# Performance work log

Hardware: AMD Instinct MI355X
Metric: run time of the kernel (lower is better)

The kernel has to match this reference:

```python
import jax, jax.numpy as jnp
import numpy as np
from jax import lax

B, N, NPOINT, NSAMPLE = 8, 8192, 2048, 32
RADIUS = 0.2
D_FEAT = 64
MLP = [64, 64, 128]
IN_CH = 3 + D_FEAT
EPS = 1e-5


def setup_inputs() -> dict:
    key = jax.random.key(0)
    ks = jax.random.split(key, 2 + len(MLP))
    inp = {
        "xyz": jax.random.uniform(ks[0], (B, N, 3), dtype=jnp.float32),
        "points": jax.random.normal(ks[1], (B, N, D_FEAT), dtype=jnp.float32),
    }
    cin = IN_CH
    for i, cout in enumerate(MLP):
        inp[f"W{i+1}"] = jax.random.normal(ks[2 + i], (cout, cin), dtype=jnp.float32) * 0.05
        inp[f"b{i+1}"] = jnp.zeros((cout,), jnp.float32)
        inp[f"g{i+1}"] = jnp.ones((cout,), jnp.float32)
        inp[f"be{i+1}"] = jnp.zeros((cout,), jnp.float32)
        cin = cout
    return inp


def farthest_point_sample(xyz, npoint):
    # xyz: (B, N, 3) -> (B, npoint) int32 indices. Deterministic start at index 0.
    Bb, Nn, _ = xyz.shape
    barange = jnp.arange(Bb)

    def step(carry, _):
        distance, farthest = carry
        centroid = xyz[barange, farthest]                      # (B, 3)
        d = jnp.sum((xyz - centroid[:, None, :]) ** 2, -1)     # (B, N)
        distance = jnp.minimum(distance, d)
        new_far = jnp.argmax(distance, axis=-1).astype(jnp.int32)
        return (distance, new_far), farthest

    init = (jnp.full((Bb, Nn), 1e10, xyz.dtype), jnp.zeros((Bb,), jnp.int32))
    _, idxs = lax.scan(step, init, None, length=npoint)        # (npoint, B)
    return idxs.T                                              # (B, npoint)


def index_points(points, idx):
    # points: (B, N, C); idx: (B, S) or (B, S, K)
    return jax.vmap(lambda p, i: p[i])(points, idx)


def square_distance(src, dst):
    # (B, S, C) x (B, N, C) -> (B, S, N)
    d = -2.0 * jnp.einsum('bsc,bnc->bsn', src, dst)
    d += jnp.sum(src ** 2, -1)[:, :, None]
    d += jnp.sum(dst ** 2, -1)[:, None, :]
    return d


def query_ball_point(radius, nsample, xyz, new_xyz):
    Bb, Nn, _ = xyz.shape
    sqr = square_distance(new_xyz, xyz)                        # (B, S, N)
    grid = jnp.arange(Nn, dtype=jnp.int32)
    group_idx = jnp.where(sqr > radius * radius, Nn, grid)     # invalid -> N
    # nsample smallest indices == torch sort(dim=-1)[:, :, :nsample]
    neg_vals, _ = lax.top_k(-group_idx, nsample)               # (B, S, K)
    group_idx = -neg_vals
    first = group_idx[:, :, 0:1]
    return jnp.where(group_idx == Nn, first, group_idx)


def bn_relu(x, gamma, beta):
    # x: (B, C, L). Training-mode batchnorm (biased variance) + ReLU.
    mean = jnp.mean(x, axis=(0, 2), keepdims=True)
    var = jnp.mean((x - mean) ** 2, axis=(0, 2), keepdims=True)
    xn = (x - mean) * lax.rsqrt(var + EPS)
    return jax.nn.relu(xn * gamma[None, :, None] + beta[None, :, None])


def reference(xyz, points, W1, b1, g1, be1, W2, b2, g2, be2, W3, b3, g3, be3):
    Bb = xyz.shape[0]
    fps_idx = farthest_point_sample(xyz, NPOINT)               # (B, S)
    new_xyz = index_points(xyz, fps_idx)                       # (B, S, 3)
    idx = query_ball_point(RADIUS, NSAMPLE, xyz, new_xyz)      # (B, S, K)
    grouped_xyz = index_points(xyz, idx)                       # (B, S, K, 3)
    grouped_xyz_norm = grouped_xyz - new_xyz[:, :, None, :]
    grouped_points = index_points(points, idx)                 # (B, S, K, D)
    g = jnp.concatenate([grouped_xyz_norm, grouped_points], -1)  # (B, S, K, C)
    x = g.reshape(Bb, NPOINT * NSAMPLE, -1).transpose(0, 2, 1)   # (B, C, S*K)
    for W, b, ga, be in ((W1, b1, g1, be1), (W2, b2, g2, be2), (W3, b3, g3, be3)):
        x = jnp.einsum('oc,bcl->bol', W, x) + b[None, :, None]
        x = bn_relu(x, ga, be)
    x = x.reshape(Bb, -1, NPOINT, NSAMPLE)
    new_points = jnp.max(x, axis=-1).transpose(0, 2, 1)        # (B, S, C_out)
    return new_xyz, new_points
```

## Files before the change

kernel.cpp:

```cpp
#include <hip/hip_runtime.h>
#include <hip/hip_bf16.h>

#define NB 8
#define NN 8192
#define NP 2048
#define NS 32
#define INV_P (1.0f/524288.0f)

typedef float v2f __attribute__((ext_vector_type(2)));

template<int CTRL>
__device__ __forceinline__ float fmax_dpp(float v) {
  const int x = __builtin_amdgcn_update_dpp(0, __float_as_int(v), CTRL, 0xF, 0xF, true);
  return fmaxf(v, __int_as_float(x));
}


__global__ __launch_bounds__(512)
void k_fps_pre(const float* __restrict__ xyz, const float* __restrict__ feat,
               const float* __restrict__ W1, const float* __restrict__ b1,
               float* __restrict__ F, float* __restrict__ outXyz, float* __restrict__ stats)
{
#pragma clang fp contract(off)
  __shared__ union U { float4 xyzw[NN]; float fx[128*64]; } sh;
  __shared__ unsigned long long cand[2][8];
  __shared__ float ctrs[3*NP];
  const int t = threadIdx.x;
  if (blockIdx.x < 8) {
    const int b = blockIdx.x;
    const float* xb = xyz + (size_t)b*NN*3;
    v2f px[8], py[8], pz[8], dd[8];
#pragma unroll
    for (int j = 0; j < 8; ++j) {
      const int i0 = t*16 + 2*j;
      const float x0 = xb[i0*3+0], y0 = xb[i0*3+1], z0 = xb[i0*3+2];
      const float x1 = xb[i0*3+3], y1 = xb[i0*3+4], z1 = xb[i0*3+5];
      px[j] = (v2f){x0,x1}; py[j] = (v2f){y0,y1}; pz[j] = (v2f){z0,z1};
      dd[j] = (v2f){1e10f,1e10f};
      sh.xyzw[i0]   = make_float4(x0,y0,z0,0.f);
      sh.xyzw[i0+1] = make_float4(x1,y1,z1,0.f);
    }
    __syncthreads();
    const int lane = t & 63, wv = t >> 6;
    float4 cf = sh.xyzw[0];
    for (int s = 0; s < NP; ++s) {
      if (t == 0) { ctrs[s] = cf.x; ctrs[NP+s] = cf.y; ctrs[2*NP+s] = cf.z; }
      const v2f cx = {cf.x,cf.x}, cy = {cf.y,cf.y}, cz = {cf.z,cf.z};
      v2f mxv = {-1.f,-1.f};
#pragma unroll
      for (int j = 0; j < 8; ++j) {
        const v2f dx = px[j]-cx, dy = py[j]-cy, dz = pz[j]-cz;
        v2f d = dx*dx; d = d + dy*dy; d = d + dz*dz;
        const v2f nd = __builtin_elementwise_min(dd[j], d);
        dd[j] = nd;
        mxv = __builtin_elementwise_max(mxv, nd);
      }
      float m = fmaxf(mxv.x, mxv.y);
      float r = m;
      r = fmax_dpp<0xB1>(r);
      r = fmax_dpp<0x4E>(r);
      r = fmax_dpp<0x141>(r);
      r = fmax_dpp<0x140>(r);
      r = fmax_dpp<0x142>(r);
      r = fmax_dpp<0x143>(r);
      const int wmb  = __builtin_amdgcn_readlane(__float_as_int(r), 63);
      const float wm = __int_as_float(wmb);
      const unsigned long long mk = __ballot(m == wm);
      const int ls = __ffsll((long long)mk) - 1;
      if (lane == ls) {
        int k = 0;
#pragma unroll
        for (int j = 7; j >= 0; --j) {
          if (dd[j].y == wm) k = 2*j+1;
          if (dd[j].x == wm) k = 2*j;
        }
        const unsigned idx = (unsigned)(t*16 + k);
        cand[s&1][wv] = ((unsigned long long)(unsigned)wmb << 32)
                      | (unsigned long long)(0xFFFFFFFFu - idx);
      }
      __syncthreads();
      unsigned long long best = cand[s&1][0];
#pragma unroll
      for (int w = 1; w < 8; ++w) { const unsigned long long c = cand[s&1][w]; if (c > best) best = c; }
      const int far = (int)(0xFFFFFFFFu - (unsigned)(best & 0xFFFFFFFFull));
      cf = sh.xyzw[far];
    }
    for (int i = t; i < NP; i += 512) {
      float* o = outXyz + ((size_t)b*NP + i)*3;
      o[0] = ctrs[i]; o[1] = ctrs[NP+i]; o[2] = ctrs[2*NP+i];
    }
  } else {
    if (blockIdx.x == 8) {
      for (int i = t; i < 512*16; i += 512) stats[i] = 0.f;
    }
    const int blk = blockIdx.x - 8;
    const int base = blk * 128;
    const int b = base >> 13;
    const int n0 = base & (NN-1);
    {
      const int row = t >> 2, seg = t & 3;
      const float* src = feat + ((size_t)(b*NN + n0 + row))*64 + seg*16;
#pragma unroll
      for (int k = 0; k < 4; ++k) {
        const float4 v = *(const float4*)(src + k*4);
        *(float4*)&sh.fx[row*64 + seg*16 + k*4] = v;
      }
    }
    __syncthreads();
    const int o = t & 63, wv = t >> 6;
    float w[64];
#pragma unroll
    for (int c = 0; c < 64; ++c) w[c] = W1[o*67 + 3 + c];
    const float bb = b1[o];
    for (int r = wv*16; r < wv*16+16; ++r) {
      float acc = bb;
#pragma unroll
      for (int c4 = 0; c4 < 16; ++c4) {
        const float4 xq = *(const float4*)&sh.fx[r*64 + c4*4];
        acc = fmaf(w[c4*4+0], xq.x, acc);
        acc = fmaf(w[c4*4+1], xq.y, acc);
        acc = fmaf(w[c4*4+2], xq.z, acc);
        acc = fmaf(w[c4*4+3], xq.w, acc);
      }
      F[((size_t)(b*NN + n0 + r))*64 + o] = acc;
    }
  }
}

__global__ __launch_bounds__(256)
void k_ball(const float* __restrict__ xyz, const float* __restrict__ newXyz,
            const float* __restrict__ F, const float* __restrict__ W1,
            __hip_bfloat16* __restrict__ y1, float* __restrict__ stats)
{
  __shared__ float xs[NN], ys[NN], zs[NN];
  __shared__ int sel[4][NS];
  const int t = threadIdx.x;
  const int b = blockIdx.x >> 5;
  const int chunk = blockIdx.x & 31;
  const float* xb = xyz + (size_t)b*NN*3;
  for (int i = t; i < NN; i += 256) {
    xs[i] = xb[i*3+0]; ys[i] = xb[i*3+1]; zs[i] = xb[i*3+2];
  }
  __syncthreads();
  const int lane = t & 63, wv = t >> 6;
  const float w0 = W1[lane*67+0], w1 = W1[lane*67+1], w2 = W1[lane*67+2];
  const double rr = 0.2*0.2;
  float ls = 0.f, lq = 0.f;
  for (int qi = 0; qi < 16; ++qi) {
    const int q  = chunk*64 + wv*16 + qi;
    const int gq = b*NP + q;
    const float cx = newXyz[(size_t)gq*3+0], cy = newXyz[(size_t)gq*3+1], cz = newXyz[(size_t)gq*3+2];
    const double cxd = (double)cx, cyd = (double)cy, czd = (double)cz;
    const double ssd = cxd*cxd + cyd*cyd + czd*czd;
    int have = 0;
    for (int c0 = 0; c0 < NN; c0 += 64) {
      const int i = c0 + lane;
      const double x = (double)xs[i], y = (double)ys[i], z = (double)zs[i];
      const double dot = x*cxd + y*cyd + z*czd;
      const double pn2 = x*x + y*y + z*z;
      const double d = -2.0*dot + ssd + pn2;
      const bool ok = d <= rr;
      const unsigned long long mk = __ballot(ok);
      const int rank = __popcll(mk & ((1ull<<lane)-1ull));
      if (ok && have + rank < NS) sel[wv][have+rank] = i;
      have += (int)__popcll(mk);
      if (have >= NS) break;
    }
    if (have > NS) have = NS;
    const int first = sel[wv][0];
    if (lane >= have && lane < NS) sel[wv][lane] = first;
    for (int j = 0; j < NS; ++j) {
      const int i = sel[wv][j];
      const float dxn = xs[i]-cx, dyn = ys[i]-cy, dzn = zs[i]-cz;
      const float f = F[((size_t)(b*NN+i))*64 + lane];
      float yv = fmaf(w0,dxn,f); yv = fmaf(w1,dyn,yv); yv = fmaf(w2,dzn,yv);
      y1[((size_t)gq*NS + j)*64 + lane] = __float2bfloat16(yv);
      ls += yv; lq = fmaf(yv,yv,lq);
    }
  }
  atomicAdd(&stats[(0 +lane)*16], ls);
  atomicAdd(&stats[(64+lane)*16], lq);
}

__device__ inline void stage_bn(const __hip_bfloat16* __restrict__ src, float* __restrict__ xt,
                                const float* __restrict__ A, const float* __restrict__ Bc,
                                int t, int blockBase)
{
  const uint4* s = (const uint4*)(src + ((size_t)(blockBase + t))*64);
  float* row = &xt[t*64];
  const int sw = t & 7;
#pragma unroll
  for (int g = 0; g < 8; ++g) {
    const uint4 v = s[g];
    const unsigned uu[4] = {v.x, v.y, v.z, v.w};
    const float4 Aq0 = ((const float4*)A)[g*2],  Aq1 = ((const float4*)A)[g*2+1];
    const float4 Bq0 = ((const float4*)Bc)[g*2], Bq1 = ((const float4*)Bc)[g*2+1];
    float e[8];
#pragma unroll
    for (int k = 0; k < 4; ++k) {
      const float f0 = __uint_as_float(uu[k] << 16);
      const float f1 = __uint_as_float(uu[k] & 0xFFFF0000u);
      const float a0 = (k<2) ? ((k==0)?Aq0.x:Aq0.z) : ((k==2)?Aq1.x:Aq1.z);
      const float a1 = (k<2) ? ((k==0)?Aq0.y:Aq0.w) : ((k==2)?Aq1.y:Aq1.w);
      const float bb0 = (k<2) ? ((k==0)?Bq0.x:Bq0.z) : ((k==2)?Bq1.x:Bq1.z);
      const float bb1 = (k<2) ? ((k==0)?Bq0.y:Bq0.w) : ((k==2)?Bq1.y:Bq1.w);
      e[k*2+0] = fmaxf(fmaf(f0, a0, bb0), 0.f);
      e[k*2+1] = fmaxf(fmaf(f1, a1, bb1), 0.f);
    }
    const float4 q0 = make_float4(e[0],e[1],e[2],e[3]);
    const float4 q1 = make_float4(e[4],e[5],e[6],e[7]);
    ((float4*)row)[(g*2)   ^ sw] = q0;
    ((float4*)row)[(g*2+1) ^ sw] = q1;
  }
}

__global__ __launch_bounds__(256)
void k_l2(const __hip_bfloat16* __restrict__ y1, float* __restrict__ stats,
          const float* __restrict__ g1, const float* __restrict__ be1,
          const float* __restrict__ W2, const float* __restrict__ b2,
          __hip_bfloat16* __restrict__ y2)
{
  __shared__ float xt[256*64];
  __shared__ float A[64], Bc[64], ssh[64], qsh[64];
  const int t = threadIdx.x;
  if (t < 64) {
    const float mean = stats[t*16] * INV_P;
    float var = stats[(64+t)*16] * INV_P - mean*mean;
    if (var < 0.f) var = 0.f;
    const float rs = rsqrtf(var + 1e-5f);
    const float a = rs * g1[t];
    A[t] = a; Bc[t] = fmaf(-mean, a, be1[t]);
    ssh[t] = 0.f; qsh[t] = 0.f;
  }
  const int lane = t & 63, wv = t >> 6;
  float w[64];
#pragma unroll
  for (int c4 = 0; c4 < 16; ++c4) {
    const float4 v = *(const float4*)(W2 + lane*64 + c4*4);
    w[c4*4+0]=v.x; w[c4*4+1]=v.y; w[c4*4+2]=v.z; w[c4*4+3]=v.w;
  }
  const float bo = b2[lane];
  __syncthreads();
  stage_bn(y1, xt, A, Bc, t, blockIdx.x*256);
  __syncthreads();
  float ls = 0.f, lq = 0.f;
  for (int pp = 0; pp < 64; ++pp) {
    const int p = wv*64 + pp;
    const int sw = p & 7;
    const float* row = &xt[p*64];
    float acc = bo;
#pragma unroll
    for (int c4 = 0; c4 < 16; ++c4) {
      const float4 xq = ((const float4*)row)[c4 ^ sw];
      acc = fmaf(w[c4*4+0], xq.x, acc);
      acc = fmaf(w[c4*4+1], xq.y, acc);
      acc = fmaf(w[c4*4+2], xq.z, acc);
      acc = fmaf(w[c4*4+3], xq.w, acc);
    }
    y2[((size_t)(blockIdx.x*256 + p))*64 + lane] = __float2bfloat16(acc);
    ls += acc; lq = fmaf(acc,acc,lq);
  }
  atomicAdd(&ssh[lane], ls);
  atomicAdd(&qsh[lane], lq);
  __syncthreads();
  if (t < 64) {
    atomicAdd(&stats[(128+t)*16], ssh[t]);
    atomicAdd(&stats[(192+t)*16], qsh[t]);
  }
}

__global__ __launch_bounds__(256)
void k_l3stats(const __hip_bfloat16* __restrict__ y2, float* __restrict__ stats,
               const float* __restrict__ g2, const float* __restrict__ be2,
               const float* __restrict__ W3, const float* __restrict__ b3)
{
  __shared__ float xt[256*64];
  __shared__ float A[64], Bc[64], ssh[128], qsh[128];
  const int t = threadIdx.x;
  if (t < 64) {
    const float mean = stats[(128+t)*16] * INV_P;
    float var = stats[(192+t)*16] * INV_P - mean*mean;
    if (var < 0.f) var = 0.f;
    const float rs = rsqrtf(var + 1e-5f);
    const float a = rs * g2[t];
    A[t] = a; Bc[t] = fmaf(-mean, a, be2[t]);
  }
  if (t < 128) { ssh[t]=0.f; qsh[t]=0.f; }
  const int lane = t & 63, wv = t >> 6;
  float w0[64], w1[64];
#pragma unroll
  for (int c4 = 0; c4 < 16; ++c4) {
    const float4 v  = *(const float4*)(W3 + lane*64 + c4*4);
    const float4 v2 = *(const float4*)(W3 + (size_t)(lane+64)*64 + c4*4);
    w0[c4*4+0]=v.x;  w0[c4*4+1]=v.y;  w0[c4*4+2]=v.z;  w0[c4*4+3]=v.w;
    w1[c4*4+0]=v2.x; w1[c4*4+1]=v2.y; w1[c4*4+2]=v2.z; w1[c4*4+3]=v2.w;
  }
  const float bo0 = b3[lane], bo1 = b3[lane+64];
  __syncthreads();
  stage_bn(y2, xt, A, Bc, t, blockIdx.x*256);
  __syncthreads();
  float ls0=0.f,lq0=0.f,ls1=0.f,lq1=0.f;
  for (int pp = 0; pp < 64; ++pp) {
    const int p = wv*64 + pp;
    const int sw = p & 7;
    const float* row = &xt[p*64];
    float a0 = bo0, a1 = bo1;
#pragma unroll
    for (int c4 = 0; c4 < 16; ++c4) {
      const float4 xq = ((const float4*)row)[c4 ^ sw];
      a0 = fmaf(w0[c4*4+0], xq.x, a0); a0 = fmaf(w0[c4*4+1], xq.y, a0);
      a0 = fmaf(w0[c4*4+2], xq.z, a0); a0 = fmaf(w0[c4*4+3], xq.w, a0);
      a1 = fmaf(w1[c4*4+0], xq.x, a1); a1 = fmaf(w1[c4*4+1], xq.y, a1);
      a1 = fmaf(w1[c4*4+2], xq.z, a1); a1 = fmaf(w1[c4*4+3], xq.w, a1);
    }
    ls0 += a0; lq0 = fmaf(a0,a0,lq0);
    ls1 += a1; lq1 = fmaf(a1,a1,lq1);
  }
  atomicAdd(&ssh[lane], ls0);    atomicAdd(&qsh[lane], lq0);
  atomicAdd(&ssh[64+lane], ls1); atomicAdd(&qsh[64+lane], lq1);
  __syncthreads();
  if (t < 128) {
    atomicAdd(&stats[(256+t)*16], ssh[t]);
    atomicAdd(&stats[(384+t)*16], qsh[t]);
  }
}

__global__ __launch_bounds__(256)
void k_out(const __hip_bfloat16* __restrict__ y2, const float* __restrict__ stats,
           const float* __restrict__ g2, const float* __restrict__ be2,
           const float* __restrict__ W3, const float* __restrict__ b3,
           const float* __restrict__ g3, const float* __restrict__ be3,
           float* __restrict__ out)
{
  __shared__ float xt[256*64];
  __shared__ float A[64], Bc[64], A3[128], B3[128];
  const int t = threadIdx.x;
  if (t < 64) {
    const float mean = stats[(128+t)*16] * INV_P;
    float var = stats[(192+t)*16] * INV_P - mean*mean;
    if (var < 0.f) var = 0.f;
    const float rs = rsqrtf(var + 1e-5f);
    const float a = rs * g2[t];
    A[t] = a; Bc[t] = fmaf(-mean, a, be2[t]);
  }
  if (t < 128) {
    const float mean = stats[(256+t)*16] * INV_P;
    float var = stats[(384+t)*16] * INV_P - mean*mean;
    if (var < 0.f) var = 0.f;
    const float rs = rsqrtf(var + 1e-5f);
    const float a = rs * g3[t];
    A3[t] = a; B3[t] = fmaf(-mean, a, be3[t]);
  }
  const int lane = t & 63, wv = t >> 6;
  float w0[64], w1[64];
#pragma unroll
  for (int c4 = 0; c4 < 16; ++c4) {
    const float4 v  = *(const float4*)(W3 + lane*64 + c4*4);
    const float4 v2 = *(const float4*)(W3 + (size_t)(lane+64)*64 + c4*4);
    w0[c4*4+0]=v.x;  w0[c4*4+1]=v.y;  w0[c4*4+2]=v.z;  w0[c4*4+3]=v.w;
    w1[c4*4+0]=v2.x; w1[c4*4+1]=v2.y; w1[c4*4+2]=v2.z; w1[c4*4+3]=v2.w;
  }
  const float bo0 = b3[lane], bo1 = b3[lane+64];
  __syncthreads();
  stage_bn(y2, xt, A, Bc, t, blockIdx.x*256);
  __syncthreads();
  const float a3l0 = A3[lane], b3l0 = B3[lane];
  const float a3l1 = A3[64+lane], b3l1 = B3[64+lane];
  for (int which = 0; which < 2; ++which) {
    float mx0 = -1e30f, mx1 = -1e30f;
    for (int j = 0; j < 32; ++j) {
      const int p = (wv*2+which)*32 + j;
      const int sw = p & 7;
      const float* row = &xt[p*64];
      float a0 = bo0, a1 = bo1;
#pragma unroll
      for (int c4 = 0; c4 < 16; ++c4) {
        const float4 xq = ((const float4*)row)[c4 ^ sw];
        a0 = fmaf(w0[c4*4+0], xq.x, a0); a0 = fmaf(w0[c4*4+1], xq.y, a0);
        a0 = fmaf(w0[c4*4+2], xq.z, a0); a0 = fmaf(w0[c4*4+3], xq.w, a0);
        a1 = fmaf(w1[c4*4+0], xq.x, a1); a1 = fmaf(w1[c4*4+1], xq.y, a1);
        a1 = fmaf(w1[c4*4+2], xq.z, a1); a1 = fmaf(w1[c4*4+3], xq.w, a1);
      }
      mx0 = fmaxf(mx0, fmaf(a0, a3l0, b3l0));
      mx1 = fmaxf(mx1, fmaf(a1, a3l1, b3l1));
    }
    const size_t gq = (size_t)blockIdx.x*8 + wv*2 + which;
    out[49152 + gq*128 + lane]      = fmaxf(mx0, 0.f);
    out[49152 + gq*128 + 64 + lane] = fmaxf(mx1, 0.f);
  }
}

extern "C" void kernel_launch(void* const* d_in, const int* in_sizes, int n_in,
                              void* d_out, int out_size, void* d_ws, size_t ws_size,
                              hipStream_t stream)
{
  const float* xyz = (const float*)d_in[0];
  const float* pts = (const float*)d_in[1];
  const float* W1  = (const float*)d_in[2];
  const float* b1  = (const float*)d_in[3];
  const float* g1  = (const float*)d_in[4];
  const float* be1 = (const float*)d_in[5];
  const float* W2  = (const float*)d_in[6];
  const float* b2_ = (const float*)d_in[7];
  const float* g2  = (const float*)d_in[8];
  const float* be2 = (const float*)d_in[9];
  const float* W3  = (const float*)d_in[10];
  const float* b3_ = (const float*)d_in[11];
  const float* g3  = (const float*)d_in[12];
  const float* be3 = (const float*)d_in[13];
  float* out = (float*)d_out;
  char* ws = (char*)d_ws;

  float* stats = (float*)(ws);
  float* F     = (float*)(ws + (1u<<20));
  __hip_bfloat16* y1 = (__hip_bfloat16*)(ws + (32u<<20));
  __hip_bfloat16* y2 = (__hip_bfloat16*)(ws + (112u<<20));

  k_fps_pre<<<520, 512, 0, stream>>>(xyz, pts, W1, b1, F, out, stats);
  k_ball<<<256, 256, 0, stream>>>(xyz, out, F, W1, y1, stats);
  k_l2<<<2048, 256, 0, stream>>>(y1, stats, g1, be1, W2, b2_, y2);
  k_l3stats<<<2048, 256, 0, stream>>>(y2, stats, g2, be2, W3, b3_);
  k_out<<<2048, 256, 0, stream>>>(y2, stats, g2, be2, W3, b3_, g3, be3, out);
}
```

Baseline: 2.505 ms.

## Shrink FPS block to four waves with 32 points per thread and winner coordinates

```diff
diff --git a/kernel.cpp b/kernel.cpp
--- a/kernel.cpp
+++ b/kernel.cpp
@@ -16,23 +16,24 @@
 }
 
 
-__global__ __launch_bounds__(512)
+__global__ __launch_bounds__(256)
 void k_fps_pre(const float* __restrict__ xyz, const float* __restrict__ feat,
                const float* __restrict__ W1, const float* __restrict__ b1,
                float* __restrict__ F, float* __restrict__ outXyz, float* __restrict__ stats)
 {
 #pragma clang fp contract(off)
-  __shared__ union U { float4 xyzw[NN]; float fx[128*64]; } sh;
-  __shared__ unsigned long long cand[2][8];
+  __shared__ union U { float4 xyzw[NN]; float fx[64*64]; } sh;
+  __shared__ unsigned long long skey[2][4];
+  __shared__ float4 scrd[2][4];
   __shared__ float ctrs[3*NP];
   const int t = threadIdx.x;
   if (blockIdx.x < 8) {
     const int b = blockIdx.x;
     const float* xb = xyz + (size_t)b*NN*3;
-    v2f px[8], py[8], pz[8], dd[8];
-#pragma unroll
-    for (int j = 0; j < 8; ++j) {
-      const int i0 = t*16 + 2*j;
+    v2f px[16], py[16], pz[16], dd[16];
+#pragma unroll
+    for (int j = 0; j < 16; ++j) {
+      const int i0 = t*32 + 2*j;
       const float x0 = xb[i0*3+0], y0 = xb[i0*3+1], z0 = xb[i0*3+2];
       const float x1 = xb[i0*3+3], y1 = xb[i0*3+4], z1 = xb[i0*3+5];
       px[j] = (v2f){x0,x1}; py[j] = (v2f){y0,y1}; pz[j] = (v2f){z0,z1};
@@ -44,18 +45,18 @@
     const int lane = t & 63, wv = t >> 6;
     float4 cf = sh.xyzw[0];
     for (int s = 0; s < NP; ++s) {
-      if (t == 0) { ctrs[s] = cf.x; ctrs[NP+s] = cf.y; ctrs[2*NP+s] = cf.z; }
+      if (t == 0) { ctrs[3*s] = cf.x; ctrs[3*s+1] = cf.y; ctrs[3*s+2] = cf.z; }
       const v2f cx = {cf.x,cf.x}, cy = {cf.y,cf.y}, cz = {cf.z,cf.z};
       v2f mxv = {-1.f,-1.f};
 #pragma unroll
-      for (int j = 0; j < 8; ++j) {
+      for (int j = 0; j < 16; ++j) {
         const v2f dx = px[j]-cx, dy = py[j]-cy, dz = pz[j]-cz;
         v2f d = dx*dx; d = d + dy*dy; d = d + dz*dz;
         const v2f nd = __builtin_elementwise_min(dd[j], d);
         dd[j] = nd;
         mxv = __builtin_elementwise_max(mxv, nd);
       }
-      float m = fmaxf(mxv.x, mxv.y);
+      const float m = fmaxf(mxv.x, mxv.y);
       float r = m;
       r = fmax_dpp<0xB1>(r);
       r = fmax_dpp<0x4E>(r);
@@ -70,31 +71,35 @@
       if (lane == ls) {
         int k = 0;
 #pragma unroll
-        for (int j = 7; j >= 0; --j) {
+        for (int j = 15; j >= 0; --j) {
           if (dd[j].y == wm) k = 2*j+1;
           if (dd[j].x == wm) k = 2*j;
         }
-        const unsigned idx = (unsigned)(t*16 + k);
-        cand[s&1][wv] = ((unsigned long long)(unsigned)wmb << 32)
+        const unsigned idx = (unsigned)(t*32 + k);
+        const float4 wc = sh.xyzw[idx];
+        skey[s&1][wv] = ((unsigned long long)(unsigned)wmb << 32)
                       | (unsigned long long)(0xFFFFFFFFu - idx);
+        scrd[s&1][wv] = wc;
       }
       __syncthreads();
-      unsigned long long best = cand[s&1][0];
-#pragma unroll
-      for (int w = 1; w < 8; ++w) { const unsigned long long c = cand[s&1][w]; if (c > best) best = c; }
-      const int far = (int)(0xFFFFFFFFu - (unsigned)(best & 0xFFFFFFFFull));
-      cf = sh.xyzw[far];
-    }
-    for (int i = t; i < NP; i += 512) {
-      float* o = outXyz + ((size_t)b*NP + i)*3;
-      o[0] = ctrs[i]; o[1] = ctrs[NP+i]; o[2] = ctrs[2*NP+i];
-    }
+      const int buf = s & 1;
+      const unsigned long long k0 = skey[buf][0], k1 = skey[buf][1];
+      const unsigned long long k2 = skey[buf][2], k3 = skey[buf][3];
+      const float4 c0 = scrd[buf][0], c1 = scrd[buf][1];
+      const float4 c2 = scrd[buf][2], c3 = scrd[buf][3];
+      unsigned long long bk = k0; float4 bc = c0;
+      if (k1 > bk) { bk = k1; bc = c1; }
+      if (k2 > bk) { bk = k2; bc = c2; }
+      if (k3 > bk) { bk = k3; bc = c3; }
+      cf = bc;
+    }
+    for (int i = t; i < 3*NP; i += 256) outXyz[(size_t)b*NP*3 + i] = ctrs[i];
   } else {
     if (blockIdx.x == 8) {
-      for (int i = t; i < 512*16; i += 512) stats[i] = 0.f;
+      for (int i = t; i < 512*16; i += 256) stats[i] = 0.f;
     }
     const int blk = blockIdx.x - 8;
-    const int base = blk * 128;
+    const int base = blk * 64;
     const int b = base >> 13;
     const int n0 = base & (NN-1);
     {
@@ -416,7 +421,7 @@
   __hip_bfloat16* y1 = (__hip_bfloat16*)(ws + (32u<<20));
   __hip_bfloat16* y2 = (__hip_bfloat16*)(ws + (112u<<20));
 
-  k_fps_pre<<<520, 512, 0, stream>>>(xyz, pts, W1, b1, F, out, stats);
+  k_fps_pre<<<1032, 256, 0, stream>>>(xyz, pts, W1, b1, F, out, stats);
   k_ball<<<256, 256, 0, stream>>>(xyz, out, F, W1, y1, stats);
   k_l2<<<2048, 256, 0, stream>>>(y1, stats, g1, be1, W2, b2_, y2);
   k_l3stats<<<2048, 256, 0, stream>>>(y2, stats, g2, be2, W3, b3_);
```

New measurement: 2.991 ms. +19.4%, slower.
